# Optimization experiments

Measured on AMD Instinct MI355X. Metric: run time of the kernel, lower is better.

## Reference

```python
import jax, jax.numpy as jnp
import numpy as np

N_HEADS = 16
D_MODEL = 1024
D_HEAD = D_MODEL // N_HEADS


def setup_inputs() -> dict:
    key = jax.random.key(0)
    k1, k2, k3, k4, k5 = jax.random.split(key, 5)
    B, S = 4, 2048
    scale = 1.0 / np.sqrt(D_MODEL)
    return {
        "x": jax.random.normal(k1, (B, S, D_MODEL), dtype=jnp.float32),
        "W_in": jax.random.normal(k2, (3 * D_MODEL, D_MODEL), dtype=jnp.float32) * scale,
        "b_in": jax.random.normal(k3, (3 * D_MODEL,), dtype=jnp.float32) * 0.02,
        "W_out": jax.random.normal(k4, (D_MODEL, D_MODEL), dtype=jnp.float32) * scale,
        "b_out": jax.random.normal(k5, (D_MODEL,), dtype=jnp.float32) * 0.02,
        "causal_mask": 1,
    }


def reference(x, W_in, b_in, W_out, b_out, causal_mask):
    b, s, d = x.shape
    # in_proj: torch Linear -> x @ W.T + b, then chunk into q,k,v
    qkv = jnp.einsum("bsd,ed->bse", x, W_in) + b_in
    q, k, v = jnp.split(qkv, 3, axis=-1)
    # [b, s, h, dh] -> [b, h, s, dh]
    q = q.reshape(b, s, N_HEADS, D_HEAD).transpose(0, 2, 1, 3)
    k = k.reshape(b, s, N_HEADS, D_HEAD).transpose(0, 2, 1, 3)
    v = v.reshape(b, s, N_HEADS, D_HEAD).transpose(0, 2, 1, 3)
    # scores [b, h, s, s]
    qk = jnp.einsum("bhqd,bhkd->bhqk", q, k)
    if causal_mask:
        mask = jnp.triu(jnp.ones((s, s), dtype=bool), k=1)
        qk = jnp.where(mask, -jnp.inf, qk)
    qk = qk / jnp.sqrt(jnp.float32(D_HEAD))
    attn = jax.nn.softmax(qk, axis=-1)
    out = jnp.einsum("bhqk,bhkd->bhqd", attn, v)  # [b, h, s, dh]
    out = out.transpose(0, 2, 1, 3).reshape(b, s, d)
    return jnp.einsum("bsd,ed->bse", out, W_out) + b_out
```

## Files before the change

kernel.cpp:

```cpp
#include <hip/hip_runtime.h>
#include <hip/hip_bf16.h>
#include <cstdint>
#include <cstddef>

typedef short bf16x8 __attribute__((ext_vector_type(8)));
typedef float f32x4 __attribute__((ext_vector_type(4)));

#define SEQ 2048
#define NH 16
#define DH 64
#define DM 1024

typedef __attribute__((address_space(1))) const void gvoid_t;
typedef __attribute__((address_space(3))) void lvoid_t;

__device__ __forceinline__ unsigned short f2bf(float f) {
  union { float f; unsigned int u; } v; v.f = f;
  return (unsigned short)((v.u + 0x7FFFu + ((v.u >> 16) & 1u)) >> 16);
}

__global__ void __launch_bounds__(256) k_cvt3(const float* __restrict__ x,
                                              const float* __restrict__ wi,
                                              const float* __restrict__ wo,
                                              unsigned short* __restrict__ xb,
                                              unsigned short* __restrict__ wib,
                                              unsigned short* __restrict__ wob) {
  int bidx = blockIdx.x;
  const float* src; unsigned short* dst; int base;
  if (bidx < 8192)       { src = x;  dst = xb;  base = bidx; }
  else if (bidx < 11264) { src = wi; dst = wib; base = bidx - 8192; }
  else                   { src = wo; dst = wob; base = bidx - 11264; }
  int i = (base * 256 + threadIdx.x) * 4;
  float4 v = *(const float4*)(src + i);
  ushort4 o;
  o.x = f2bf(v.x); o.y = f2bf(v.y); o.z = f2bf(v.z); o.w = f2bf(v.w);
  *(ushort4*)(dst + i) = o;
}

__device__ __forceinline__ void gemm_tile_bt(const unsigned short* __restrict__ A,
                                             const unsigned short* __restrict__ Bt,
                                             unsigned short* lA, unsigned short* lB,
                                             int m0, int n0, f32x4 (&acc)[4][4]) {
  const int t = threadIdx.x;
  const int wave = t >> 6, lane = t & 63, quad = lane >> 4, l16 = lane & 15;
  const int mh = (wave >> 1) * 64, nh = (wave & 1) * 64;
  int row_[4], c_[4];
#pragma unroll
  for (int r = 0; r < 4; ++r) {
    int i = r * 256 + t;
    row_[r] = i >> 3;
    c_[r] = ((i & 7) ^ ((i >> 3) & 7)) * 8;
  }
  const int sw0 = ((quad) ^ (l16 & 7)) * 8;
  const int sw1 = ((quad ^ 4) ^ (l16 & 7)) * 8;
  for (int k0 = 0; k0 < DM; k0 += 64) {
    __syncthreads();
#pragma unroll
    for (int r = 0; r < 4; ++r) {
      __builtin_amdgcn_global_load_lds((gvoid_t*)&A[(size_t)(m0 + row_[r]) * DM + k0 + c_[r]],
                                       (lvoid_t*)&lA[(r * 4 + wave) * 512], 16, 0, 0);
      __builtin_amdgcn_global_load_lds((gvoid_t*)&Bt[(size_t)(n0 + row_[r]) * DM + k0 + c_[r]],
                                       (lvoid_t*)&lB[(r * 4 + wave) * 512], 16, 0, 0);
    }
    __syncthreads();
    bf16x8 af[4], bfr[4];
#pragma unroll
    for (int i = 0; i < 4; ++i)
      af[i] = *(const bf16x8*)(&lA[(mh + i * 16 + l16) * 64 + sw0]);
#pragma unroll
    for (int i = 0; i < 4; ++i)
      bfr[i] = *(const bf16x8*)(&lB[(nh + i * 16 + l16) * 64 + sw0]);
#pragma unroll
    for (int mt = 0; mt < 4; ++mt)
#pragma unroll
      for (int nt = 0; nt < 4; ++nt)
        acc[mt][nt] = __builtin_amdgcn_mfma_f32_16x16x32_bf16(af[mt], bfr[nt], acc[mt][nt], 0, 0, 0);
#pragma unroll
    for (int i = 0; i < 4; ++i)
      af[i] = *(const bf16x8*)(&lA[(mh + i * 16 + l16) * 64 + sw1]);
#pragma unroll
    for (int i = 0; i < 4; ++i)
      bfr[i] = *(const bf16x8*)(&lB[(nh + i * 16 + l16) * 64 + sw1]);
#pragma unroll
    for (int mt = 0; mt < 4; ++mt)
#pragma unroll
      for (int nt = 0; nt < 4; ++nt)
        acc[mt][nt] = __builtin_amdgcn_mfma_f32_16x16x32_bf16(af[mt], bfr[nt], acc[mt][nt], 0, 0, 0);
  }
}

__global__ void __launch_bounds__(256, 2) k_gemm_qkv(
    const unsigned short* __restrict__ X,
    const unsigned short* __restrict__ Wi,
    const float* __restrict__ bias,
    unsigned short* __restrict__ Qo,
    unsigned short* __restrict__ Ko,
    unsigned short* __restrict__ Vto) {
  __shared__ unsigned short lA[128 * 64];
  __shared__ unsigned short lB[128 * 64];
  const int t = threadIdx.x;
  const int wave = t >> 6, lane = t & 63, quad = lane >> 4, l16 = lane & 15;
  const int m0 = blockIdx.x * 128, n0 = blockIdx.y * 128;
  f32x4 acc[4][4];
  f32x4 zf = {0.f, 0.f, 0.f, 0.f};
  for (int i = 0; i < 4; ++i)
    for (int j = 0; j < 4; ++j) acc[i][j] = zf;
  gemm_tile_bt(X, Wi, lA, lB, m0, n0, acc);

  const int mh = (wave >> 1) * 64, nh = (wave & 1) * 64;
  const float SCALE = 0.18033688011112042f;
#pragma unroll
  for (int nt = 0; nt < 4; ++nt) {
    int gcol = n0 + nh + nt * 16 + l16;
    float bv = bias[gcol];
    if (gcol < 1024) {
      int hh = gcol >> 6, dh = gcol & 63;
#pragma unroll
      for (int mt = 0; mt < 4; ++mt) {
        int rowbase = m0 + mh + mt * 16 + quad * 4;
        int bb = rowbase >> 11, sb = rowbase & 2047;
#pragma unroll
        for (int r = 0; r < 4; ++r)
          Qo[((size_t)(bb * NH + hh) * SEQ + sb + r) * DH + dh] =
              f2bf((acc[mt][nt][r] + bv) * SCALE);
      }
    } else if (gcol < 2048) {
      int c = gcol - 1024; int hh = c >> 6, dh = c & 63;
#pragma unroll
      for (int mt = 0; mt < 4; ++mt) {
        int rowbase = m0 + mh + mt * 16 + quad * 4;
        int bb = rowbase >> 11, sb = rowbase & 2047;
#pragma unroll
        for (int r = 0; r < 4; ++r)
          Ko[((size_t)(bb * NH + hh) * SEQ + sb + r) * DH + dh] = f2bf(acc[mt][nt][r] + bv);
      }
    } else {
      int c = gcol - 2048; int hh = c >> 6, dh = c & 63;
#pragma unroll
      for (int mt = 0; mt < 4; ++mt) {
        int rowbase = m0 + mh + mt * 16 + quad * 4;
        int bb = rowbase >> 11, sb = rowbase & 2047;
        ushort4 pk;
        pk.x = f2bf(acc[mt][nt][0] + bv);
        pk.y = f2bf(acc[mt][nt][1] + bv);
        pk.z = f2bf(acc[mt][nt][2] + bv);
        pk.w = f2bf(acc[mt][nt][3] + bv);
        *(ushort4*)(&Vto[((size_t)(bb * NH + hh) * DH + dh) * SEQ + sb]) = pk;
      }
    }
  }
}

#define ASTR 72

__global__ void __launch_bounds__(256, 4) k_attn(
    const unsigned short* __restrict__ Q,
    const unsigned short* __restrict__ K,
    const unsigned short* __restrict__ Vt,
    unsigned short* __restrict__ Ao,
    const int* __restrict__ causal_p) {
  __shared__ unsigned short lK[64 * 64];
  __shared__ unsigned short lV[64 * 64];
  __shared__ unsigned short lP[2][4][16 * ASTR];

  const int t = threadIdx.x;
  const int wave = t >> 6, lane = t & 63, quad = lane >> 4, l16 = lane & 15;
  const int x = blockIdx.x, h = blockIdx.y, b = blockIdx.z;
  const int qtA = x, qtB = 31 - x;
  const int bh = b * NH + h;
  const int causal = causal_p[0];
  const int ktA = causal ? qtA : 31;
  const int ktB = causal ? qtB : 31;
  const int q0A = qtA * 64, q0B = qtB * 64;

  const unsigned short* Qb = Q + (size_t)bh * SEQ * DH;
  const unsigned short* Kb = K + (size_t)bh * SEQ * DH;
  const unsigned short* Vb = Vt + (size_t)bh * DH * SEQ;

  bf16x8 qA0 = *(const bf16x8*)(&Qb[(q0A + wave * 16 + l16) * DH + quad * 8]);
  bf16x8 qA1 = *(const bf16x8*)(&Qb[(q0A + wave * 16 + l16) * DH + 32 + quad * 8]);
  bf16x8 qB0 = *(const bf16x8*)(&Qb[(q0B + wave * 16 + l16) * DH + quad * 8]);
  bf16x8 qB1 = *(const bf16x8*)(&Qb[(q0B + wave * 16 + l16) * DH + 32 + quad * 8]);

  f32x4 zf = {0.f, 0.f, 0.f, 0.f};
  f32x4 oA[4], oB[4];
  for (int i = 0; i < 4; ++i) { oA[i] = zf; oB[i] = zf; }
  f32x4 lacA = zf, lacB = zf;

  bf16x8 ones;
#pragma unroll
  for (int i = 0; i < 8; ++i) ones[i] = (short)0x3F80;

  unsigned short* lPa = &lP[0][wave][0];
  unsigned short* lPb = &lP[1][wave][0];

  const int i0 = t, i1 = 256 + t;
  const int rr0 = i0 >> 3, cc0 = ((i0 & 7) ^ (rr0 & 7)) * 8;
  const int rr1 = i1 >> 3, cc1 = ((i1 & 7) ^ (rr1 & 7)) * 8;
  const int kof0 = rr0 * DH + cc0, kof1 = rr1 * DH + cc1;
  const int vof0 = rr0 * SEQ + cc0, vof1 = rr1 * SEQ + cc1;
  const int rbase = l16 * 64;
  const int sw0 = ((quad ^ (l16 & 7)) * 8);
  const int sw1 = (((quad ^ 4) ^ (l16 & 7)) * 8);

  for (int kt = 0; kt <= ktB; ++kt) {
    const int k0 = kt * 64;
    const bool doA = (kt <= ktA);

    __syncthreads();
    __builtin_amdgcn_global_load_lds((gvoid_t*)(Kb + (size_t)k0 * DH + kof0),
                                     (lvoid_t*)&lK[wave * 512], 16, 0, 0);
    __builtin_amdgcn_global_load_lds((gvoid_t*)(Kb + (size_t)k0 * DH + kof1),
                                     (lvoid_t*)&lK[wave * 512 + 2048], 16, 0, 0);
    __builtin_amdgcn_global_load_lds((gvoid_t*)(Vb + k0 + vof0),
                                     (lvoid_t*)&lV[wave * 512], 16, 0, 0);
    __builtin_amdgcn_global_load_lds((gvoid_t*)(Vb + k0 + vof1),
                                     (lvoid_t*)&lV[wave * 512 + 2048], 16, 0, 0);
    __syncthreads();

    f32x4 sA[4], sB[4];
#pragma unroll
    for (int nt = 0; nt < 4; ++nt) {
      bf16x8 kf0 = *(const bf16x8*)(&lK[nt * 1024 + rbase + sw0]);
      bf16x8 kf1 = *(const bf16x8*)(&lK[nt * 1024 + rbase + sw1]);
      f32x4 zb = zf;
      zb = __builtin_amdgcn_mfma_f32_16x16x32_bf16(qB0, kf0, zb, 0, 0, 0);
      zb = __builtin_amdgcn_mfma_f32_16x16x32_bf16(qB1, kf1, zb, 0, 0, 0);
      sB[nt] = zb;
      if (doA) {
        f32x4 za = zf;
        za = __builtin_amdgcn_mfma_f32_16x16x32_bf16(qA0, kf0, za, 0, 0, 0);
        za = __builtin_amdgcn_mfma_f32_16x16x32_bf16(qA1, kf1, za, 0, 0, 0);
        sA[nt] = za;
      }
    }

    if (causal && kt == qtB) {
#pragma unroll
      for (int nt = 0; nt < 4; ++nt) {
        int kcol = k0 + nt * 16 + l16;
#pragma unroll
        for (int r = 0; r < 4; ++r)
          if (kcol > q0B + wave * 16 + quad * 4 + r) sB[nt][r] = -1e30f;
      }
    }
    if (causal && doA && kt == qtA) {
#pragma unroll
      for (int nt = 0; nt < 4; ++nt) {
        int kcol = k0 + nt * 16 + l16;
#pragma unroll
        for (int r = 0; r < 4; ++r)
          if (kcol > q0A + wave * 16 + quad * 4 + r) sA[nt][r] = -1e30f;
      }
    }

#pragma unroll
    for (int nt = 0; nt < 4; ++nt)
#pragma unroll
      for (int r = 0; r < 4; ++r)
        lPb[(quad * 4 + r) * ASTR + nt * 16 + l16] =
            f2bf(__builtin_amdgcn_exp2f(sB[nt][r]));
    if (doA) {
#pragma unroll
      for (int nt = 0; nt < 4; ++nt)
#pragma unroll
        for (int r = 0; r < 4; ++r)
          lPa[(quad * 4 + r) * ASTR + nt * 16 + l16] =
              f2bf(__builtin_amdgcn_exp2f(sA[nt][r]));
    }

    asm volatile("s_waitcnt lgkmcnt(0)" ::: "memory");

    bf16x8 pB0 = *(const bf16x8*)(&lPb[l16 * ASTR + quad * 8]);
    bf16x8 pB1 = *(const bf16x8*)(&lPb[l16 * ASTR + 32 + quad * 8]);
    bf16x8 pA0 = pB0, pA1 = pB1;
    if (doA) {
      pA0 = *(const bf16x8*)(&lPa[l16 * ASTR + quad * 8]);
      pA1 = *(const bf16x8*)(&lPa[l16 * ASTR + 32 + quad * 8]);
    }

    lacB = __builtin_amdgcn_mfma_f32_16x16x32_bf16(pB0, ones, lacB, 0, 0, 0);
    lacB = __builtin_amdgcn_mfma_f32_16x16x32_bf16(pB1, ones, lacB, 0, 0, 0);
    if (doA) {
      lacA = __builtin_amdgcn_mfma_f32_16x16x32_bf16(pA0, ones, lacA, 0, 0, 0);
      lacA = __builtin_amdgcn_mfma_f32_16x16x32_bf16(pA1, ones, lacA, 0, 0, 0);
    }

#pragma unroll
    for (int nt = 0; nt < 4; ++nt) {
      bf16x8 vf0 = *(const bf16x8*)(&lV[nt * 1024 + rbase + sw0]);
      bf16x8 vf1 = *(const bf16x8*)(&lV[nt * 1024 + rbase + sw1]);
      oB[nt] = __builtin_amdgcn_mfma_f32_16x16x32_bf16(pB0, vf0, oB[nt], 0, 0, 0);
      oB[nt] = __builtin_amdgcn_mfma_f32_16x16x32_bf16(pB1, vf1, oB[nt], 0, 0, 0);
      if (doA) {
        oA[nt] = __builtin_amdgcn_mfma_f32_16x16x32_bf16(pA0, vf0, oA[nt], 0, 0, 0);
        oA[nt] = __builtin_amdgcn_mfma_f32_16x16x32_bf16(pA1, vf1, oA[nt], 0, 0, 0);
      }
    }
  }

#pragma unroll
  for (int r = 0; r < 4; ++r) {
    float invB = 1.0f / lacB[r];
    float invA = 1.0f / lacA[r];
#pragma unroll
    for (int nt = 0; nt < 4; ++nt) {
      int dh = nt * 16 + l16;
      int qgB = q0B + wave * 16 + quad * 4 + r;
      Ao[(size_t)(b * SEQ + qgB) * DM + h * DH + dh] = f2bf(oB[nt][r] * invB);
      int qgA = q0A + wave * 16 + quad * 4 + r;
      Ao[(size_t)(b * SEQ + qgA) * DM + h * DH + dh] = f2bf(oA[nt][r] * invA);
    }
  }
}

__global__ void __launch_bounds__(256, 2) k_gemm_out(
    const unsigned short* __restrict__ Ai,
    const unsigned short* __restrict__ Wo,
    const float* __restrict__ bias,
    float* __restrict__ C) {
  __shared__ unsigned short lA[128 * 64];
  __shared__ unsigned short lB[128 * 64];
  const int t = threadIdx.x;
  const int wave = t >> 6, lane = t & 63, quad = lane >> 4, l16 = lane & 15;
  const int m0 = blockIdx.x * 128, n0 = blockIdx.y * 128;
  f32x4 acc[4][4];
  f32x4 zf = {0.f, 0.f, 0.f, 0.f};
  for (int i = 0; i < 4; ++i)
    for (int j = 0; j < 4; ++j) acc[i][j] = zf;
  gemm_tile_bt(Ai, Wo, lA, lB, m0, n0, acc);
  const int mh = (wave >> 1) * 64, nh = (wave & 1) * 64;
#pragma unroll
  for (int nt = 0; nt < 4; ++nt) {
    int gcol = n0 + nh + nt * 16 + l16;
    float bv = bias[gcol];
#pragma unroll
    for (int mt = 0; mt < 4; ++mt) {
      int rowbase = m0 + mh + mt * 16 + quad * 4;
#pragma unroll
      for (int r = 0; r < 4; ++r)
        C[(size_t)(rowbase + r) * DM + gcol] = acc[mt][nt][r] + bv;
    }
  }
}

extern "C" void kernel_launch(void* const* d_in, const int* in_sizes, int n_in,
                              void* d_out, int out_size, void* d_ws, size_t ws_size,
                              hipStream_t stream) {
  (void)in_sizes; (void)n_in; (void)out_size; (void)ws_size;
  const float* x     = (const float*)d_in[0];
  const float* W_in  = (const float*)d_in[1];
  const float* b_in  = (const float*)d_in[2];
  const float* W_out = (const float*)d_in[3];
  const float* b_out = (const float*)d_in[4];
  const int* causal  = (const int*)d_in[5];
  float* out = (float*)d_out;
  char* ws = (char*)d_ws;

  unsigned short* xb  = (unsigned short*)(ws + 0);
  unsigned short* Aob = (unsigned short*)(ws + 0);
  unsigned short* Wib = (unsigned short*)(ws + (size_t)(16 << 20));
  unsigned short* Wob = (unsigned short*)(ws + (size_t)(22 << 20));
  unsigned short* Qb  = (unsigned short*)(ws + (size_t)(24 << 20));
  unsigned short* Kb  = (unsigned short*)(ws + (size_t)(40 << 20));
  unsigned short* Vtb = (unsigned short*)(ws + (size_t)(56 << 20));

  k_cvt3<<<12288, 256, 0, stream>>>(x, W_in, W_out, xb, Wib, Wob);
  k_gemm_qkv<<<dim3(64, 24), 256, 0, stream>>>(xb, Wib, b_in, Qb, Kb, Vtb);
  k_attn<<<dim3(16, 16, 4), 256, 0, stream>>>(Qb, Kb, Vtb, Aob, causal);
  k_gemm_out<<<dim3(64, 8), 256, 0, stream>>>(Aob, Wob, b_out, out);
}
```

Before: 245.4 us.

## Rewrite projection GEMMs as 256x256 double-buffered pipelined tiles with 8 waves

Replaces the 128x128, 4-wave GEMM core used by the QKV and output projections with a 256x256 tile computed by 8 waves. Global-to-LDS loads are double-buffered and interleaved in half-tiles with MFMA quadrants, using explicit barriers, vmcnt/lgkmcnt waits and s_setprio. Workgroup IDs are swizzled for L2 locality. This aims to hide load latency and raise data reuse per tile. The cost is higher register pressure and far fewer workgroups: 128 for the output GEMM, which may underfill 256 CUs.

```diff
diff --git a/kernel.cpp b/kernel.cpp
--- a/kernel.cpp
+++ b/kernel.cpp
@@ -37,114 +37,202 @@
   *(ushort4*)(dst + i) = o;
 }
 
-__device__ __forceinline__ void gemm_tile_bt(const unsigned short* __restrict__ A,
-                                             const unsigned short* __restrict__ Bt,
-                                             unsigned short* lA, unsigned short* lB,
-                                             int m0, int n0, f32x4 (&acc)[4][4]) {
+#define LDS_T 16384
+
+__device__ __forceinline__ void barx() {
+  asm volatile("" ::: "memory");
+  __builtin_amdgcn_s_barrier();
+  asm volatile("" ::: "memory");
+}
+#define LGKM0() asm volatile("s_waitcnt lgkmcnt(0)" ::: "memory")
+#define VMC4()  asm volatile("s_waitcnt vmcnt(4)" ::: "memory")
+
+__device__ __forceinline__ void stage_half(const unsigned short* __restrict__ G,
+                                           int row0, int kt, unsigned short* lds,
+                                           int Rhalf, int rstat, int cOff, int wave) {
+#pragma unroll
+  for (int pc = 0; pc < 2; ++pc) {
+    const int R = Rhalf + pc * 64;
+    __builtin_amdgcn_global_load_lds(
+        (gvoid_t*)(G + (size_t)(row0 + R + rstat) * DM + kt * 64 + cOff),
+        (lvoid_t*)(lds + (R + wave * 8) * 64), 16, 0, 0);
+  }
+}
+
+__device__ __forceinline__ void lda8(const unsigned short* lds, int rb, int l16,
+                                     int sw0, int sw1, bf16x8 (&a)[8]) {
+#pragma unroll
+  for (int f = 0; f < 4; ++f) {
+    const unsigned short* p = lds + (rb + f * 16 + l16) * 64;
+    a[f * 2 + 0] = *(const bf16x8*)(p + sw0);
+    a[f * 2 + 1] = *(const bf16x8*)(p + sw1);
+  }
+}
+
+__device__ __forceinline__ void ldb4(const unsigned short* lds, int rb, int l16,
+                                     int sw0, int sw1, bf16x8 (&b)[4]) {
+#pragma unroll
+  for (int g = 0; g < 2; ++g) {
+    const unsigned short* p = lds + (rb + g * 16 + l16) * 64;
+    b[g * 2 + 0] = *(const bf16x8*)(p + sw0);
+    b[g * 2 + 1] = *(const bf16x8*)(p + sw1);
+  }
+}
+
+template <int MQ, int NQ>
+__device__ __forceinline__ void mfma_quad(const bf16x8 (&a)[8], const bf16x8 (&b)[4],
+                                          f32x4 (&acc)[8][4]) {
+  __builtin_amdgcn_s_setprio(1);
+#pragma unroll
+  for (int f = 0; f < 4; ++f)
+#pragma unroll
+    for (int g = 0; g < 2; ++g) {
+      f32x4 c = acc[MQ * 4 + f][NQ * 2 + g];
+      c = __builtin_amdgcn_mfma_f32_16x16x32_bf16(a[f * 2 + 0], b[g * 2 + 0], c, 0, 0, 0);
+      c = __builtin_amdgcn_mfma_f32_16x16x32_bf16(a[f * 2 + 1], b[g * 2 + 1], c, 0, 0, 0);
+      acc[MQ * 4 + f][NQ * 2 + g] = c;
+    }
+  __builtin_amdgcn_s_setprio(0);
+}
+
+__device__ __forceinline__ void gemm256(const unsigned short* __restrict__ A,
+                                        const unsigned short* __restrict__ Bt,
+                                        unsigned short* lA, unsigned short* lB,
+                                        int m0, int n0, f32x4 (&acc)[8][4]) {
   const int t = threadIdx.x;
   const int wave = t >> 6, lane = t & 63, quad = lane >> 4, l16 = lane & 15;
-  const int mh = (wave >> 1) * 64, nh = (wave & 1) * 64;
-  int row_[4], c_[4];
-#pragma unroll
-  for (int r = 0; r < 4; ++r) {
-    int i = r * 256 + t;
-    row_[r] = i >> 3;
-    c_[r] = ((i & 7) ^ ((i >> 3) & 7)) * 8;
-  }
-  const int sw0 = ((quad) ^ (l16 & 7)) * 8;
+  const int wm = wave >> 2, wn = wave & 3;
+  const int rstat = t >> 3;
+  const int cOff = ((t & 7) ^ (rstat & 7)) * 8;
+  const int sw0 = (quad ^ (l16 & 7)) * 8;
   const int sw1 = ((quad ^ 4) ^ (l16 & 7)) * 8;
-  for (int k0 = 0; k0 < DM; k0 += 64) {
-    __syncthreads();
-#pragma unroll
-    for (int r = 0; r < 4; ++r) {
-      __builtin_amdgcn_global_load_lds((gvoid_t*)&A[(size_t)(m0 + row_[r]) * DM + k0 + c_[r]],
-                                       (lvoid_t*)&lA[(r * 4 + wave) * 512], 16, 0, 0);
-      __builtin_amdgcn_global_load_lds((gvoid_t*)&Bt[(size_t)(n0 + row_[r]) * DM + k0 + c_[r]],
-                                       (lvoid_t*)&lB[(r * 4 + wave) * 512], 16, 0, 0);
-    }
-    __syncthreads();
-    bf16x8 af[4], bfr[4];
-#pragma unroll
-    for (int i = 0; i < 4; ++i)
-      af[i] = *(const bf16x8*)(&lA[(mh + i * 16 + l16) * 64 + sw0]);
-#pragma unroll
-    for (int i = 0; i < 4; ++i)
-      bfr[i] = *(const bf16x8*)(&lB[(nh + i * 16 + l16) * 64 + sw0]);
-#pragma unroll
-    for (int mt = 0; mt < 4; ++mt)
-#pragma unroll
-      for (int nt = 0; nt < 4; ++nt)
-        acc[mt][nt] = __builtin_amdgcn_mfma_f32_16x16x32_bf16(af[mt], bfr[nt], acc[mt][nt], 0, 0, 0);
-#pragma unroll
-    for (int i = 0; i < 4; ++i)
-      af[i] = *(const bf16x8*)(&lA[(mh + i * 16 + l16) * 64 + sw1]);
-#pragma unroll
-    for (int i = 0; i < 4; ++i)
-      bfr[i] = *(const bf16x8*)(&lB[(nh + i * 16 + l16) * 64 + sw1]);
-#pragma unroll
-    for (int mt = 0; mt < 4; ++mt)
-#pragma unroll
-      for (int nt = 0; nt < 4; ++nt)
-        acc[mt][nt] = __builtin_amdgcn_mfma_f32_16x16x32_bf16(af[mt], bfr[nt], acc[mt][nt], 0, 0, 0);
-  }
-}
-
-__global__ void __launch_bounds__(256, 2) k_gemm_qkv(
+  const int arb0 = wm * 64, arb1 = 128 + wm * 64;
+  const int brb0 = wn * 32, brb1 = 128 + wn * 32;
+  const int NT = DM / 64;
+
+  bf16x8 af[8], b0[4], b1[4];
+
+  stage_half(A,  m0, 0, lA, 0,   rstat, cOff, wave);
+  stage_half(Bt, n0, 0, lB, 0,   rstat, cOff, wave);
+  stage_half(A,  m0, 0, lA, 128, rstat, cOff, wave);
+  stage_half(Bt, n0, 0, lB, 128, rstat, cOff, wave);
+  stage_half(A,  m0, 1, lA + LDS_T, 0,   rstat, cOff, wave);
+  stage_half(Bt, n0, 1, lB + LDS_T, 128, rstat, cOff, wave);
+  VMC4();
+  barx();
+
+  for (int t0 = 0; t0 < NT; t0 += 2) {
+    const int t2 = (t0 + 2 < NT) ? t0 + 2 : NT - 1;
+    const int t3 = (t0 + 3 < NT) ? t0 + 3 : NT - 1;
+    lda8(lA, arb0, l16, sw0, sw1, af);
+    ldb4(lB, brb0, l16, sw0, sw1, b0);
+    stage_half(A, m0, t0 + 1, lA + LDS_T, 128, rstat, cOff, wave);
+    barx(); LGKM0();
+    mfma_quad<0, 0>(af, b0, acc);
+    barx();
+    ldb4(lB, brb1, l16, sw0, sw1, b1);
+    stage_half(Bt, n0, t0 + 1, lB + LDS_T, 0, rstat, cOff, wave);
+    barx(); LGKM0();
+    mfma_quad<0, 1>(af, b1, acc);
+    barx();
+    lda8(lA, arb1, l16, sw0, sw1, af);
+    stage_half(A, m0, t2, lA, 0, rstat, cOff, wave);
+    barx(); LGKM0();
+    mfma_quad<1, 1>(af, b1, acc);
+    barx();
+    stage_half(Bt, n0, t2, lB, 128, rstat, cOff, wave);
+    VMC4();
+    barx(); LGKM0();
+    mfma_quad<1, 0>(af, b0, acc);
+    barx();
+    lda8(lA + LDS_T, arb0, l16, sw0, sw1, af);
+    ldb4(lB + LDS_T, brb0, l16, sw0, sw1, b0);
+    stage_half(A, m0, t2, lA, 128, rstat, cOff, wave);
+    barx(); LGKM0();
+    mfma_quad<0, 0>(af, b0, acc);
+    barx();
+    ldb4(lB + LDS_T, brb1, l16, sw0, sw1, b1);
+    stage_half(Bt, n0, t2, lB, 0, rstat, cOff, wave);
+    barx(); LGKM0();
+    mfma_quad<0, 1>(af, b1, acc);
+    barx();
+    lda8(lA + LDS_T, arb1, l16, sw0, sw1, af);
+    stage_half(A, m0, t3, lA + LDS_T, 0, rstat, cOff, wave);
+    barx(); LGKM0();
+    mfma_quad<1, 1>(af, b1, acc);
+    barx();
+    stage_half(Bt, n0, t3, lB + LDS_T, 128, rstat, cOff, wave);
+    VMC4();
+    barx(); LGKM0();
+    mfma_quad<1, 0>(af, b0, acc);
+    barx();
+  }
+}
+
+__global__ void __launch_bounds__(512, 2) k_gemm_qkv(
     const unsigned short* __restrict__ X,
     const unsigned short* __restrict__ Wi,
     const float* __restrict__ bias,
     unsigned short* __restrict__ Qo,
     unsigned short* __restrict__ Ko,
     unsigned short* __restrict__ Vto) {
-  __shared__ unsigned short lA[128 * 64];
-  __shared__ unsigned short lB[128 * 64];
+  __shared__ unsigned short lA[2 * LDS_T];
+  __shared__ unsigned short lB[2 * LDS_T];
   const int t = threadIdx.x;
   const int wave = t >> 6, lane = t & 63, quad = lane >> 4, l16 = lane & 15;
-  const int m0 = blockIdx.x * 128, n0 = blockIdx.y * 128;
-  f32x4 acc[4][4];
+  const int wm = wave >> 2, wn = wave & 3;
+  const int nwg = 32 * 12;
+  const int bid = blockIdx.x;
+  const int swz = (bid & 7) * (nwg / 8) + (bid >> 3);
+  const int m0 = (swz / 12) * 256, n0 = (swz % 12) * 256;
+
+  f32x4 acc[8][4];
   f32x4 zf = {0.f, 0.f, 0.f, 0.f};
-  for (int i = 0; i < 4; ++i)
+#pragma unroll
+  for (int i = 0; i < 8; ++i)
+#pragma unroll
     for (int j = 0; j < 4; ++j) acc[i][j] = zf;
-  gemm_tile_bt(X, Wi, lA, lB, m0, n0, acc);
-
-  const int mh = (wave >> 1) * 64, nh = (wave & 1) * 64;
+
+  gemm256(X, Wi, lA, lB, m0, n0, acc);
+
   const float SCALE = 0.18033688011112042f;
-#pragma unroll
-  for (int nt = 0; nt < 4; ++nt) {
-    int gcol = n0 + nh + nt * 16 + l16;
-    float bv = bias[gcol];
-    if (gcol < 1024) {
-      int hh = gcol >> 6, dh = gcol & 63;
-#pragma unroll
-      for (int mt = 0; mt < 4; ++mt) {
-        int rowbase = m0 + mh + mt * 16 + quad * 4;
-        int bb = rowbase >> 11, sb = rowbase & 2047;
+  const int sel = n0 >> 10;
+#pragma unroll
+  for (int nf = 0; nf < 4; ++nf) {
+    const int gcol = n0 + (nf >> 1) * 128 + wn * 32 + (nf & 1) * 16 + l16;
+    const float bv = bias[gcol];
+    const int c = gcol & 1023;
+    const int hh = c >> 6, dh = c & 63;
+    if (sel == 0) {
+#pragma unroll
+      for (int mf = 0; mf < 8; ++mf) {
+        const int grow = m0 + (mf >> 2) * 128 + wm * 64 + (mf & 3) * 16 + quad * 4;
+        const int bb = grow >> 11, sb = grow & 2047;
+        unsigned short* qp = Qo + ((size_t)(bb * NH + hh) * SEQ + sb) * DH + dh;
 #pragma unroll
         for (int r = 0; r < 4; ++r)
-          Qo[((size_t)(bb * NH + hh) * SEQ + sb + r) * DH + dh] =
-              f2bf((acc[mt][nt][r] + bv) * SCALE);
-      }
-    } else if (gcol < 2048) {
-      int c = gcol - 1024; int hh = c >> 6, dh = c & 63;
-#pragma unroll
-      for (int mt = 0; mt < 4; ++mt) {
-        int rowbase = m0 + mh + mt * 16 + quad * 4;
-        int bb = rowbase >> 11, sb = rowbase & 2047;
+          qp[(size_t)r * DH] = f2bf((acc[mf][nf][r] + bv) * SCALE);
+      }
+    } else if (sel == 1) {
+#pragma unroll
+      for (int mf = 0; mf < 8; ++mf) {
+        const int grow = m0 + (mf >> 2) * 128 + wm * 64 + (mf & 3) * 16 + quad * 4;
+        const int bb = grow >> 11, sb = grow & 2047;
+        unsigned short* kp = Ko + ((size_t)(bb * NH + hh) * SEQ + sb) * DH + dh;
 #pragma unroll
         for (int r = 0; r < 4; ++r)
-          Ko[((size_t)(bb * NH + hh) * SEQ + sb + r) * DH + dh] = f2bf(acc[mt][nt][r] + bv);
+          kp[(size_t)r * DH] = f2bf(acc[mf][nf][r] + bv);
       }
     } else {
-      int c = gcol - 2048; int hh = c >> 6, dh = c & 63;
-#pragma unroll
-      for (int mt = 0; mt < 4; ++mt) {
-        int rowbase = m0 + mh + mt * 16 + quad * 4;
-        int bb = rowbase >> 11, sb = rowbase & 2047;
+#pragma unroll
+      for (int mf = 0; mf < 8; ++mf) {
+        const int grow = m0 + (mf >> 2) * 128 + wm * 64 + (mf & 3) * 16 + quad * 4;
+        const int bb = grow >> 11, sb = grow & 2047;
         ushort4 pk;
-        pk.x = f2bf(acc[mt][nt][0] + bv);
-        pk.y = f2bf(acc[mt][nt][1] + bv);
-        pk.z = f2bf(acc[mt][nt][2] + bv);
-        pk.w = f2bf(acc[mt][nt][3] + bv);
+        pk.x = f2bf(acc[mf][nf][0] + bv);
+        pk.y = f2bf(acc[mf][nf][1] + bv);
+        pk.z = f2bf(acc[mf][nf][2] + bv);
+        pk.w = f2bf(acc[mf][nf][3] + bv);
         *(ushort4*)(&Vto[((size_t)(bb * NH + hh) * DH + dh) * SEQ + sb]) = pk;
       }
     }
@@ -314,32 +402,39 @@
   }
 }
 
-__global__ void __launch_bounds__(256, 2) k_gemm_out(
+__global__ void __launch_bounds__(512, 2) k_gemm_out(
     const unsigned short* __restrict__ Ai,
     const unsigned short* __restrict__ Wo,
     const float* __restrict__ bias,
     float* __restrict__ C) {
-  __shared__ unsigned short lA[128 * 64];
-  __shared__ unsigned short lB[128 * 64];
+  __shared__ unsigned short lA[2 * LDS_T];
+  __shared__ unsigned short lB[2 * LDS_T];
   const int t = threadIdx.x;
   const int wave = t >> 6, lane = t & 63, quad = lane >> 4, l16 = lane & 15;
-  const int m0 = blockIdx.x * 128, n0 = blockIdx.y * 128;
-  f32x4 acc[4][4];
+  const int wm = wave >> 2, wn = wave & 3;
+  const int bid = blockIdx.x;
+  const int swz = (bid & 7) * 16 + (bid >> 3);
+  const int m0 = (swz >> 2) * 256, n0 = (swz & 3) * 256;
+
+  f32x4 acc[8][4];
   f32x4 zf = {0.f, 0.f, 0.f, 0.f};
-  for (int i = 0; i < 4; ++i)
+#pragma unroll
+  for (int i = 0; i < 8; ++i)
+#pragma unroll
     for (int j = 0; j < 4; ++j) acc[i][j] = zf;
-  gemm_tile_bt(Ai, Wo, lA, lB, m0, n0, acc);
-  const int mh = (wave >> 1) * 64, nh = (wave & 1) * 64;
-#pragma unroll
-  for (int nt = 0; nt < 4; ++nt) {
-    int gcol = n0 + nh + nt * 16 + l16;
-    float bv = bias[gcol];
-#pragma unroll
-    for (int mt = 0; mt < 4; ++mt) {
-      int rowbase = m0 + mh + mt * 16 + quad * 4;
+
+  gemm256(Ai, Wo, lA, lB, m0, n0, acc);
+
+#pragma unroll
+  for (int nf = 0; nf < 4; ++nf) {
+    const int gcol = n0 + (nf >> 1) * 128 + wn * 32 + (nf & 1) * 16 + l16;
+    const float bv = bias[gcol];
+#pragma unroll
+    for (int mf = 0; mf < 8; ++mf) {
+      const int grow = m0 + (mf >> 2) * 128 + wm * 64 + (mf & 3) * 16 + quad * 4;
 #pragma unroll
       for (int r = 0; r < 4; ++r)
-        C[(size_t)(rowbase + r) * DM + gcol] = acc[mt][nt][r] + bv;
+        C[(size_t)(grow + r) * DM + gcol] = acc[mf][nf][r] + bv;
     }
   }
 }
@@ -366,7 +461,7 @@
   unsigned short* Vtb = (unsigned short*)(ws + (size_t)(56 << 20));
 
   k_cvt3<<<12288, 256, 0, stream>>>(x, W_in, W_out, xb, Wib, Wob);
-  k_gemm_qkv<<<dim3(64, 24), 256, 0, stream>>>(xb, Wib, b_in, Qb, Kb, Vtb);
+  k_gemm_qkv<<<384, 512, 0, stream>>>(xb, Wib, b_in, Qb, Kb, Vtb);
   k_attn<<<dim3(16, 16, 4), 256, 0, stream>>>(Qb, Kb, Vtb, Aob, causal);
-  k_gemm_out<<<dim3(64, 8), 256, 0, stream>>>(Aob, Wob, b_out, out);
-}
+  k_gemm_out<<<128, 512, 0, stream>>>(Aob, Wob, b_out, out);
+}
```

After: 262.1 us. 6.8% more time.
